# Optimization experiments

Measured on AMD Instinct MI355X. Metric: run time of the kernel, lower is better.

The kernel has to match this reference:

```python
import jax, jax.numpy as jnp
import numpy as np

SIGMA1 = 0.1  # init kwarg s


def setup_inputs() -> dict:
    key = jax.random.key(0)
    k1, k2 = jax.random.split(key)
    N, D = 8192, 128
    fvec = jax.random.normal(k1, (N, D), dtype=jnp.float32)
    Lvec = jax.random.randint(k2, (N,), 0, 1024, dtype=jnp.int32)
    a = jnp.ones((), dtype=jnp.float32)
    return {"fvec": fvec, "Lvec": Lvec, "a": a, "IPC": 512, "bz": 8192}


def reference(fvec, Lvec, a, IPC, bz):
    # data != 'SOP' branch of HSELoss.forward (Lvec is unused on this path).
    N = fvec.shape[0]
    # F.normalize(fvec, p=2, dim=1) with eps clamp
    norm = jnp.maximum(jnp.linalg.norm(fvec, axis=1, keepdims=True), 1e-12)
    fn = fvec / norm
    # distMC: cosine-sim matmul with diagonal forced to -1
    idx = jnp.arange(N)
    Dist = (fn @ fn.T).at[idx, idx].set(-1.0)  # [N, N]

    Dd = jax.lax.stop_gradient(Dist)  # D_detach clones
    rows = idx[:, None]
    cols = idx[None, :]
    row_sel = (rows >= bz - IPC) & (rows < bz)
    # easy: mask cols [2*IPC, bz) on the last IPC rows
    easy = jnp.where(row_sel & (cols >= 2 * IPC) & (cols < bz), -1.0, Dd)
    # hard: mask cols [0, 2*IPC) and [bz-IPC, bz) on the last IPC rows
    hard_cols = (cols < 2 * IPC) | ((cols >= bz - IPC) & (cols < bz))
    hard = jnp.where(row_sel & hard_cols, -1.0, Dd)

    I_easy = jnp.argmax(easy, axis=1)  # first max index, matches torch .max(1)
    I_hard = jnp.argmax(hard, axis=1)
    VCE = Dist[idx, I_easy]
    VCH = Dist[idx, I_hard]
    T1 = jnp.stack([VCE, VCH], axis=1)[-IPC:]  # [IPC, 2]
    Prob1 = -jax.nn.log_softmax(T1 / SIGMA1, axis=1)[:, 0]
    return a * Prob1.mean()
```

## Files before the change

kernel.cpp:

```cpp
#include <hip/hip_runtime.h>
#include <hip/hip_bf16.h>
#include <math.h>

constexpr int N   = 8192;
constexpr int D   = 128;
constexpr int IPC = 512;
constexpr int BZ  = 8192;
constexpr int Q0  = BZ - IPC;
constexpr int NQ  = IPC;
constexpr int JMAX = BZ - IPC;
constexpr int JBLK = 128;
constexpr int NJB  = JMAX / JBLK;
constexpr int EASY_JB = (2 * IPC) / JBLK;
constexpr int QBLK = 64;
constexpr int NQB  = NQ / QBLK;
constexpr int RSTR = 136;

typedef __attribute__((ext_vector_type(8))) short short8;
typedef __attribute__((ext_vector_type(4))) float f32x4;

__global__ __launch_bounds__(256) void kmain(const float* __restrict__ f,
                                             float* __restrict__ pm) {
    __shared__ __align__(16) short S[192 * RSTR];
    __shared__ float red[4][QBLK];

    const int tid  = threadIdx.x;
    const int lane = tid & 63;
    const int wv   = tid >> 6;
    const int jblk = blockIdx.x;
    const int qblk = blockIdx.y;

    {
        const int sub = tid & 15;
        const int rof = tid >> 4;
        #pragma unroll
        for (int i = 0; i < 12; ++i) {
            int ridx = i * 16 + rof;
            int grow = (ridx < QBLK) ? (Q0 + qblk * QBLK + ridx)
                                     : (jblk * JBLK + (ridx - QBLK));
            const float* rp = f + (size_t)grow * D + sub * 8;
            float4 v0 = *(const float4*)(rp);
            float4 v1 = *(const float4*)(rp + 4);
            float ss = v0.x*v0.x + v0.y*v0.y + v0.z*v0.z + v0.w*v0.w
                     + v1.x*v1.x + v1.y*v1.y + v1.z*v1.z + v1.w*v1.w;
            #pragma unroll
            for (int off = 1; off < 16; off <<= 1) ss += __shfl_xor(ss, off, 64);
            float r = 1.0f / fmaxf(sqrtf(ss), 1e-12f);
            float sc[8] = { v0.x*r, v0.y*r, v0.z*r, v0.w*r,
                            v1.x*r, v1.y*r, v1.z*r, v1.w*r };
            short8 h;
            #pragma unroll
            for (int e = 0; e < 8; ++e) {
                __hip_bfloat16 b = __float2bfloat16(sc[e]);
                h[e] = *(short*)&b;
            }
            *(short8*)&S[ridx * RSTR + sub * 8] = h;
        }
    }
    __syncthreads();

    const int row16 = lane & 15;
    const int kgrp  = lane >> 4;
    const short* As = S;
    const short* Bs = S + QBLK * RSTR + wv * 32 * RSTR;

    f32x4 acc[4][2] = {};
    #pragma unroll
    for (int c = 0; c < 4; ++c) {
        const int ko = c * 32 + kgrp * 8;
        short8 a[4], b[2];
        #pragma unroll
        for (int g = 0; g < 4; ++g)
            a[g] = *(const short8*)(As + (g * 16 + row16) * RSTR + ko);
        #pragma unroll
        for (int t = 0; t < 2; ++t)
            b[t] = *(const short8*)(Bs + (t * 16 + row16) * RSTR + ko);
        #pragma unroll
        for (int g = 0; g < 4; ++g)
            #pragma unroll
            for (int t = 0; t < 2; ++t)
                acc[g][t] = __builtin_amdgcn_mfma_f32_16x16x32_bf16(a[g], b[t], acc[g][t], 0, 0, 0);
    }

    float vg[4][4];
    #pragma unroll
    for (int g = 0; g < 4; ++g)
        #pragma unroll
        for (int r = 0; r < 4; ++r)
            vg[g][r] = fmaxf(acc[g][0][r], acc[g][1][r]);
    #pragma unroll
    for (int off = 1; off < 16; off <<= 1)
        #pragma unroll
        for (int g = 0; g < 4; ++g)
            #pragma unroll
            for (int r = 0; r < 4; ++r)
                vg[g][r] = fmaxf(vg[g][r], __shfl_xor(vg[g][r], off, 64));

    if ((lane & 15) == 0) {
        int sgrp = lane >> 4;
        #pragma unroll
        for (int g = 0; g < 4; ++g)
            #pragma unroll
            for (int r = 0; r < 4; ++r)
                red[wv][g * 16 + sgrp * 4 + r] = vg[g][r];
    }
    __syncthreads();
    if (tid < QBLK) {
        float m = fmaxf(fmaxf(red[0][tid], red[1][tid]),
                        fmaxf(red[2][tid], red[3][tid]));
        pm[(size_t)(qblk * QBLK + tid) * NJB + jblk] = m;
    }
}

__global__ __launch_bounds__(512) void kfinal(const float* __restrict__ pm,
                                              const float* __restrict__ a_in,
                                              float* __restrict__ out) {
    __shared__ float wsum[8];
    int q = threadIdx.x;
    const float* row = pm + (size_t)q * NJB;
    float vce = -1e30f, vch = -1e30f;
    #pragma unroll
    for (int c = 0; c < EASY_JB; ++c) vce = fmaxf(vce, row[c]);
    #pragma unroll
    for (int c = EASY_JB; c < NJB; ++c) vch = fmaxf(vch, row[c]);
    float d = (vch - vce) * 10.0f;
    float p = (d > 0.0f) ? (d + log1pf(expf(-d))) : log1pf(expf(d));
    #pragma unroll
    for (int off = 32; off > 0; off >>= 1) p += __shfl_xor(p, off, 64);
    int lane = q & 63, w = q >> 6;
    if (lane == 0) wsum[w] = p;
    __syncthreads();
    if (q == 0) {
        float s = 0.0f;
        #pragma unroll
        for (int i = 0; i < 8; ++i) s += wsum[i];
        out[0] = a_in[0] * (s / (float)NQ);
    }
}

extern "C" void kernel_launch(void* const* d_in, const int* in_sizes, int n_in,
                              void* d_out, int out_size, void* d_ws, size_t ws_size,
                              hipStream_t stream) {
    const float* f = (const float*)d_in[0];
    const float* a = (const float*)d_in[2];

    float* pm  = (float*)d_ws;
    float* out = (float*)d_out;

    dim3 g(NJB, NQB);
    kmain<<<g, 256, 0, stream>>>(f, pm);
    kfinal<<<1, 512, 0, stream>>>(pm, a, out);
}
```

Before: 71.72 us.

## Defer L2 normalization to post-MFMA scaling and vectorize final reduction

Rows are converted to bf16 without normalization. Their squared norms are batched into one set of shuffle reductions and the reciprocal norms are stored in shared memory. Column and row reciprocal norms are applied to the MFMA outputs before the max, so the per-row serial shuffle-then-scale dependency before the LDS write goes away. The final kernel reads partial maxima with float4 loads, and launch bounds now ask for two blocks per CU. Casting unnormalized values to bf16 changes rounding slightly relative to normalizing first.

```diff
diff --git a/kernel.cpp b/kernel.cpp
--- a/kernel.cpp
+++ b/kernel.cpp
@@ -19,9 +19,10 @@
 typedef __attribute__((ext_vector_type(8))) short short8;
 typedef __attribute__((ext_vector_type(4))) float f32x4;
 
-__global__ __launch_bounds__(256) void kmain(const float* __restrict__ f,
-                                             float* __restrict__ pm) {
+__global__ __launch_bounds__(256, 2) void kmain(const float* __restrict__ f,
+                                                float* __restrict__ pm) {
     __shared__ __align__(16) short S[192 * RSTR];
+    __shared__ float Rn[192];
     __shared__ float red[4][QBLK];
 
     const int tid  = threadIdx.x;
@@ -33,6 +34,7 @@
     {
         const int sub = tid & 15;
         const int rof = tid >> 4;
+        float ssr[12];
         #pragma unroll
         for (int i = 0; i < 12; ++i) {
             int ridx = i * 16 + rof;
@@ -41,20 +43,26 @@
             const float* rp = f + (size_t)grow * D + sub * 8;
             float4 v0 = *(const float4*)(rp);
             float4 v1 = *(const float4*)(rp + 4);
-            float ss = v0.x*v0.x + v0.y*v0.y + v0.z*v0.z + v0.w*v0.w
-                     + v1.x*v1.x + v1.y*v1.y + v1.z*v1.z + v1.w*v1.w;
+            __hip_bfloat162 b0 = __float22bfloat162_rn({v0.x, v0.y});
+            __hip_bfloat162 b1 = __float22bfloat162_rn({v0.z, v0.w});
+            __hip_bfloat162 b2 = __float22bfloat162_rn({v1.x, v1.y});
+            __hip_bfloat162 b3 = __float22bfloat162_rn({v1.z, v1.w});
+            uint4 hw;
+            hw.x = *(unsigned*)&b0;
+            hw.y = *(unsigned*)&b1;
+            hw.z = *(unsigned*)&b2;
+            hw.w = *(unsigned*)&b3;
+            *(uint4*)&S[ridx * RSTR + sub * 8] = hw;
+            ssr[i] = v0.x*v0.x + v0.y*v0.y + v0.z*v0.z + v0.w*v0.w
+                   + v1.x*v1.x + v1.y*v1.y + v1.z*v1.z + v1.w*v1.w;
+        }
+        #pragma unroll
+        for (int off = 1; off < 16; off <<= 1)
             #pragma unroll
-            for (int off = 1; off < 16; off <<= 1) ss += __shfl_xor(ss, off, 64);
-            float r = 1.0f / fmaxf(sqrtf(ss), 1e-12f);
-            float sc[8] = { v0.x*r, v0.y*r, v0.z*r, v0.w*r,
-                            v1.x*r, v1.y*r, v1.z*r, v1.w*r };
-            short8 h;
-            #pragma unroll
-            for (int e = 0; e < 8; ++e) {
-                __hip_bfloat16 b = __float2bfloat16(sc[e]);
-                h[e] = *(short*)&b;
-            }
-            *(short8*)&S[ridx * RSTR + sub * 8] = h;
+            for (int i = 0; i < 12; ++i) ssr[i] += __shfl_xor(ssr[i], off, 64);
+        if (sub < 12) {
+            int ridx = sub * 16 + rof;
+            Rn[ridx] = 1.0f / fmaxf(sqrtf(ssr[sub]), 1e-12f);
         }
     }
     __syncthreads();
@@ -82,12 +90,14 @@
                 acc[g][t] = __builtin_amdgcn_mfma_f32_16x16x32_bf16(a[g], b[t], acc[g][t], 0, 0, 0);
     }
 
+    float rj0 = Rn[QBLK + wv * 32 + row16];
+    float rj1 = Rn[QBLK + wv * 32 + 16 + row16];
     float vg[4][4];
     #pragma unroll
     for (int g = 0; g < 4; ++g)
         #pragma unroll
         for (int r = 0; r < 4; ++r)
-            vg[g][r] = fmaxf(acc[g][0][r], acc[g][1][r]);
+            vg[g][r] = fmaxf(acc[g][0][r] * rj0, acc[g][1][r] * rj1);
     #pragma unroll
     for (int off = 1; off < 16; off <<= 1)
         #pragma unroll
@@ -108,7 +118,7 @@
     if (tid < QBLK) {
         float m = fmaxf(fmaxf(red[0][tid], red[1][tid]),
                         fmaxf(red[2][tid], red[3][tid]));
-        pm[(size_t)(qblk * QBLK + tid) * NJB + jblk] = m;
+        pm[(size_t)(qblk * QBLK + tid) * NJB + jblk] = m * Rn[tid];
     }
 }
 
@@ -117,12 +127,18 @@
                                               float* __restrict__ out) {
     __shared__ float wsum[8];
     int q = threadIdx.x;
-    const float* row = pm + (size_t)q * NJB;
+    const float4* row = (const float4*)(pm + (size_t)q * NJB);
     float vce = -1e30f, vch = -1e30f;
     #pragma unroll
-    for (int c = 0; c < EASY_JB; ++c) vce = fmaxf(vce, row[c]);
+    for (int c = 0; c < EASY_JB / 4; ++c) {
+        float4 v = row[c];
+        vce = fmaxf(fmaxf(vce, fmaxf(v.x, v.y)), fmaxf(v.z, v.w));
+    }
     #pragma unroll
-    for (int c = EASY_JB; c < NJB; ++c) vch = fmaxf(vch, row[c]);
+    for (int c = EASY_JB / 4; c < NJB / 4; ++c) {
+        float4 v = row[c];
+        vch = fmaxf(fmaxf(vch, fmaxf(v.x, v.y)), fmaxf(v.z, v.w));
+    }
     float d = (vch - vce) * 10.0f;
     float p = (d > 0.0f) ? (d + log1pf(expf(-d))) : log1pf(expf(d));
     #pragma unroll
```

Result: slower. 73.58 us (+2.6%).
